# Performance work log

Measured on AMD Instinct MI355X. Metric: run time of the kernel, lower is better.

The kernel has to match this reference:

```python
import jax, jax.numpy as jnp
import numpy as np

SOBEL_X = jnp.array([[-1., 0., 1.], [-2., 0., 2.], [-1., 0., 1.]], dtype=jnp.float32).reshape(1, 1, 3, 3)
SOBEL_Y = jnp.array([[-1., -2., -1.], [0., 0., 0.], [1., 2., 1.]], dtype=jnp.float32).reshape(1, 1, 3, 3)
KERNEL_MASK = jnp.ones((1, 1, 3, 3), dtype=jnp.float32)


def _conv(x, k):
    # x: (N,1,H,W), k: (1,1,3,3), SAME padding (matches torch padding=1)
    return jax.lax.conv_general_dilated(
        x, k, window_strides=(1, 1), padding='SAME',
        dimension_numbers=('NCHW', 'OIHW', 'NCHW'))


def setup_inputs() -> dict:
    key = jax.random.key(0)
    k1, k2, k3 = jax.random.split(key, 3)
    shape = (2, 6, 512, 512, 8)  # (B, T, H, W, F)
    prediction = jax.random.normal(k1, shape, dtype=jnp.float32)
    target = jax.random.normal(k2, shape, dtype=jnp.float32)
    mask = jax.random.randint(k3, shape, 0, 2, dtype=jnp.int32)
    return {"prediction": prediction, "target": target, "mask": mask}


def reference(prediction, target, mask):
    B, T, H, W, F = prediction.shape
    # (B,T,H,W,F) -> (B*T*F, 1, H, W)
    def to_nchw(x):
        return x.transpose(0, 1, 4, 2, 3).reshape(B * T * F, 1, H, W)

    mask_r = to_nchw(mask.astype(jnp.float32))
    pred_r = to_nchw(prediction)
    tgt_r = to_nchw(target)

    valid = (_conv(mask_r, KERNEL_MASK) == 9.0).astype(prediction.dtype)

    gx_p = _conv(pred_r, SOBEL_X) * valid
    gy_p = _conv(pred_r, SOBEL_Y) * valid
    gx_t = _conv(tgt_r, SOBEL_X) * valid
    gy_t = _conv(tgt_r, SOBEL_Y) * valid

    # mode == 'l1'
    loss = jnp.abs(gx_p - gx_t) + jnp.abs(gy_p - gy_t)
    # (B*T*F,1,H,W) -> (B,T,H,W,F)
    return loss.reshape(B, T, F, H, W).transpose(0, 1, 3, 4, 2)
```

## Files before the change

kernel.cpp:

```cpp
#include <hip/hip_runtime.h>


constexpr int H = 512, W = 512, F = 8;
constexpr int IMAGES = 12;
constexpr int SEG_H = 8;
constexpr int SEGS = H / SEG_H;
constexpr int STRIPS = 18;
constexpr int ROWE = W * F;
constexpr size_t IMG_ELEMS = (size_t)H * W * F;

__device__ __forceinline__ float4 sub4(float4 a, float4 b) {
    return make_float4(a.x - b.x, a.y - b.y, a.z - b.z, a.w - b.w);
}

__device__ __forceinline__ float4 shfl4(float4 v, int src) {
    float4 r;
    r.x = __shfl(v.x, src, 64);
    r.y = __shfl(v.y, src, 64);
    r.z = __shfl(v.z, src, 64);
    r.w = __shfl(v.w, src, 64);
    return r;
}

struct RowRaw { float4 p, t; int4 m; };

__device__ __forceinline__ RowRaw load_row(const float* __restrict__ pred,
                                           const float* __restrict__ tgt,
                                           const int*   __restrict__ mask,
                                           size_t colbase, int h) {
    const int hc = min(max(h, 0), H - 1);
    const size_t off = colbase + (size_t)hc * ROWE;
    RowRaw r;
    r.p = *(const float4*)(pred + off);
    r.t = *(const float4*)(tgt + off);
    r.m = *(const int4*)(mask + off);
    return r;
}

__device__ __forceinline__ void fold(const RowRaw& r, int hval, bool gpin,
                                     float4& d, unsigned& mv) {
    d = sub4(r.p, r.t);
    const unsigned pk = (unsigned)(r.m.x | (r.m.y << 1) | (r.m.z << 2) | (r.m.w << 3));
    mv = (hval >= 0 && hval < H && gpin) ? pk : 0u;
}

__global__ __launch_bounds__(256) void sobel_loss_kernel(
    const float* __restrict__ pred,
    const float* __restrict__ tgt,
    const int*   __restrict__ mask,
    float*       __restrict__ out)
{
    const int lane = threadIdx.x & 63;
    const int wid  = (blockIdx.x << 2) + (threadIdx.x >> 6);
    const int seg  = wid & (SEGS - 1);
    const int t2   = wid >> 6;
    const int strip = t2 % STRIPS;
    const int img   = t2 / STRIPS;

    const int h0 = seg * SEG_H;
    const int ws = strip * 30;
    const int p  = lane >> 1;
    const int qq = lane & 1;
    const int gp = ws - 1 + p;
    const bool gpin = (gp >= 0) & (gp < W);
    const int gpc = min(max(gp, 0), W - 1);
    const size_t ibase = (size_t)img * IMG_ELEMS;
    const size_t colbase = ibase + (size_t)gpc * F + qq * 4;

    float4 dm1, d0c, dp1;
    unsigned mm1, m0c, mp1;
    {
        RowRaw r = load_row(pred, tgt, mask, colbase, h0 - 1);
        fold(r, h0 - 1, gpin, dm1, mm1);
        r = load_row(pred, tgt, mask, colbase, h0);
        fold(r, h0, gpin, d0c, m0c);
        r = load_row(pred, tgt, mask, colbase, h0 + 1);
        fold(r, h0 + 1, gpin, dp1, mp1);
    }
    RowRaw stageA = load_row(pred, tgt, mask, colbase, h0 + 2);
    RowRaw stageB = load_row(pred, tgt, mask, colbase, h0 + 3);

    const bool do_store = (p >= 1) & (p < 31) & (gp < W);
    const int lm2 = lane - 2, lp2 = lane + 2;
    const int hmax = h0 + SEG_H;

    float* const outcol = out + ibase + (size_t)gp * F + qq * 4;

    auto step = [&](int h, RowRaw& stage) {
        const float4 v1 = make_float4(fmaf(2.f, d0c.x, dm1.x) + dp1.x,
                                      fmaf(2.f, d0c.y, dm1.y) + dp1.y,
                                      fmaf(2.f, d0c.z, dm1.z) + dp1.z,
                                      fmaf(2.f, d0c.w, dm1.w) + dp1.w);
        const float4 v2 = sub4(dp1, dm1);
        const unsigned mvv = mm1 & m0c & mp1;

        const float4 v1l = shfl4(v1, lm2), v1r = shfl4(v1, lp2);
        const float4 v2l = shfl4(v2, lm2), v2r = shfl4(v2, lp2);
        const unsigned ml = (unsigned)__shfl((int)mvv, lm2, 64);
        const unsigned mr = (unsigned)__shfl((int)mvv, lp2, 64);
        const unsigned valid = mvv & ml & mr;

        float4 res;
        res.x = (valid & 1u) ? fabsf(v1r.x - v1l.x) + fabsf(fmaf(2.f, v2.x, v2l.x) + v2r.x) : 0.f;
        res.y = (valid & 2u) ? fabsf(v1r.y - v1l.y) + fabsf(fmaf(2.f, v2.y, v2l.y) + v2r.y) : 0.f;
        res.z = (valid & 4u) ? fabsf(v1r.z - v1l.z) + fabsf(fmaf(2.f, v2.z, v2l.z) + v2r.z) : 0.f;
        res.w = (valid & 8u) ? fabsf(v1r.w - v1l.w) + fabsf(fmaf(2.f, v2.w, v2l.w) + v2r.w) : 0.f;

        if (do_store)
            *(float4*)(outcol + (size_t)h * ROWE) = res;

        dm1 = d0c; mm1 = m0c;
        d0c = dp1; m0c = mp1;
        fold(stage, h + 2, gpin, dp1, mp1);
        stage = load_row(pred, tgt, mask, colbase, min(h + 4, hmax));
    };

#pragma unroll
    for (int h = h0; h < hmax; h += 2) {
        step(h,     stageA);
        step(h + 1, stageB);
    }
}

extern "C" void kernel_launch(void* const* d_in, const int* in_sizes, int n_in,
                              void* d_out, int out_size, void* d_ws, size_t ws_size,
                              hipStream_t stream) {
    const float* pred = (const float*)d_in[0];
    const float* tgt  = (const float*)d_in[1];
    const int*   mask = (const int*)d_in[2];
    float*       out  = (float*)d_out;

    const int blocks = IMAGES * STRIPS * SEGS / 4;
    sobel_loss_kernel<<<blocks, 256, 0, stream>>>(pred, tgt, mask, out);
}
```

Measured before the change: 307.6 us.

## Double segment height and deepen row prefetch to three staged rows

Each wavefront now processes 16 rows instead of 8, so fewer halo rows are re-read per output row and the launch has half as many wavefronts. The prefetch pipeline grows from two staged rows to three, keeping more loads in flight. Redundant tail loads are skipped. The cost is more registers per thread and fewer wavefronts, which may lower occupancy and the ability to hide latency.

```diff
diff --git a/kernel.cpp b/kernel.cpp
--- a/kernel.cpp
+++ b/kernel.cpp
@@ -3,7 +3,7 @@
 
 constexpr int H = 512, W = 512, F = 8;
 constexpr int IMAGES = 12;
-constexpr int SEG_H = 8;
+constexpr int SEG_H = 16;
 constexpr int SEGS = H / SEG_H;
 constexpr int STRIPS = 18;
 constexpr int ROWE = W * F;
@@ -53,7 +53,7 @@
     const int lane = threadIdx.x & 63;
     const int wid  = (blockIdx.x << 2) + (threadIdx.x >> 6);
     const int seg  = wid & (SEGS - 1);
-    const int t2   = wid >> 6;
+    const int t2   = wid >> 5;
     const int strip = t2 % STRIPS;
     const int img   = t2 / STRIPS;
 
@@ -67,26 +67,29 @@
     const size_t ibase = (size_t)img * IMG_ELEMS;
     const size_t colbase = ibase + (size_t)gpc * F + qq * 4;
 
+    RowRaw r0 = load_row(pred, tgt, mask, colbase, h0 - 1);
+    RowRaw r1 = load_row(pred, tgt, mask, colbase, h0);
+    RowRaw r2 = load_row(pred, tgt, mask, colbase, h0 + 1);
+    RowRaw s0 = load_row(pred, tgt, mask, colbase, h0 + 2);
+    RowRaw s1 = load_row(pred, tgt, mask, colbase, h0 + 3);
+    RowRaw s2 = load_row(pred, tgt, mask, colbase, h0 + 4);
+
     float4 dm1, d0c, dp1;
     unsigned mm1, m0c, mp1;
-    {
-        RowRaw r = load_row(pred, tgt, mask, colbase, h0 - 1);
-        fold(r, h0 - 1, gpin, dm1, mm1);
-        r = load_row(pred, tgt, mask, colbase, h0);
-        fold(r, h0, gpin, d0c, m0c);
-        r = load_row(pred, tgt, mask, colbase, h0 + 1);
-        fold(r, h0 + 1, gpin, dp1, mp1);
-    }
-    RowRaw stageA = load_row(pred, tgt, mask, colbase, h0 + 2);
-    RowRaw stageB = load_row(pred, tgt, mask, colbase, h0 + 3);
+    fold(r0, h0 - 1, gpin, dm1, mm1);
+    fold(r1, h0,     gpin, d0c, m0c);
+    fold(r2, h0 + 1, gpin, dp1, mp1);
 
     const bool do_store = (p >= 1) & (p < 31) & (gp < W);
     const int lm2 = lane - 2, lp2 = lane + 2;
-    const int hmax = h0 + SEG_H;
 
     float* const outcol = out + ibase + (size_t)gp * F + qq * 4;
 
-    auto step = [&](int h, RowRaw& stage) {
+#pragma unroll
+    for (int k = 0; k < SEG_H; ++k) {
+        const int h = h0 + k;
+        RowRaw& st = (k % 3 == 0) ? s0 : (k % 3 == 1) ? s1 : s2;
+
         const float4 v1 = make_float4(fmaf(2.f, d0c.x, dm1.x) + dp1.x,
                                       fmaf(2.f, d0c.y, dm1.y) + dp1.y,
                                       fmaf(2.f, d0c.z, dm1.z) + dp1.z,
@@ -109,16 +112,14 @@
         if (do_store)
             *(float4*)(outcol + (size_t)h * ROWE) = res;
 
-        dm1 = d0c; mm1 = m0c;
-        d0c = dp1; m0c = mp1;
-        fold(stage, h + 2, gpin, dp1, mp1);
-        stage = load_row(pred, tgt, mask, colbase, min(h + 4, hmax));
-    };
-
-#pragma unroll
-    for (int h = h0; h < hmax; h += 2) {
-        step(h,     stageA);
-        step(h + 1, stageB);
+        if (k < SEG_H - 1) {
+            dm1 = d0c; mm1 = m0c;
+            d0c = dp1; m0c = mp1;
+            fold(st, h + 2, gpin, dp1, mp1);
+        }
+        if (k <= SEG_H - 5) {
+            st = load_row(pred, tgt, mask, colbase, h + 5);
+        }
     }
 }
 
```

New measurement: 316.2 us. 2.8% more time.
